# Kernel tuning notes

Hardware: AMD Instinct MI355X
Metric: run time of the kernel (lower is better)

Reference implementation:

```python
import jax, jax.numpy as jnp
import numpy as np

B, L, F = 32, 8192, 16
R, S = 32, 32            # residual / skip channels
NUM_BLOCKS, NUM_LAYERS = 3, 4
DILATIONS = [2 ** (i + j * NUM_LAYERS) for j in range(NUM_BLOCKS) for i in range(NUM_LAYERS)]  # 1..2048


def conv1d(x, w, b, dilation=1, padding=0):
    # x: (N, C, L), w: (O, I, K), matches torch Conv1d semantics
    y = jax.lax.conv_general_dilated(
        x, w, window_strides=(1,), padding=[(padding, padding)],
        rhs_dilation=(dilation,), dimension_numbers=("NCH", "OIH", "NCH"))
    return y + b[None, :, None]


def setup_inputs() -> dict:
    key = jax.random.key(0)
    ks = jax.random.split(key, 16)
    nl = NUM_BLOCKS * NUM_LAYERS
    sd = 0.1
    return {
        "x": jax.random.normal(ks[0], (B, L, F), dtype=jnp.float32),
        "in_w": sd * jax.random.normal(ks[1], (R, F, 1), dtype=jnp.float32),
        "in_b": jnp.zeros((R,), jnp.float32),
        "dil_w": sd * jax.random.normal(ks[2], (nl, 2 * R, R, 2), dtype=jnp.float32),
        "dil_b": jnp.zeros((nl, 2 * R), jnp.float32),
        "skip_w": sd * jax.random.normal(ks[3], (nl, S, R, 1), dtype=jnp.float32),
        "skip_b": jnp.zeros((nl, S), jnp.float32),
        "res_w": sd * jax.random.normal(ks[4], (nl, R, R, 1), dtype=jnp.float32),
        "res_b": jnp.zeros((nl, R), jnp.float32),
        "f1_w": sd * jax.random.normal(ks[5], (S, S, 1), dtype=jnp.float32),
        "f1_b": jnp.zeros((S,), jnp.float32),
        "f2_w": sd * jax.random.normal(ks[6], (1, S, 1), dtype=jnp.float32),
        "f2_b": jnp.zeros((1,), jnp.float32),
    }


def reference(x, in_w, in_b, dil_w, dil_b, skip_w, skip_b, res_w, res_b, f1_w, f1_b, f2_w, f2_b):
    # (B, L, F) -> (B, F, L)
    h = conv1d(jnp.transpose(x, (0, 2, 1)), in_w, in_b)
    skip_sum = None
    for l, d in enumerate(DILATIONS):
        residual = h
        y = conv1d(h, dil_w[l], dil_b[l], dilation=d, padding=d // 2)
        gate, filt = y[:, :R], y[:, R:]  # torch.chunk(dim=1)
        h = jnp.tanh(filt) * jax.nn.sigmoid(gate)
        s = conv1d(h, skip_w[l], skip_b[l])
        skip_sum = s if skip_sum is None else skip_sum + s
        h = conv1d(h, res_w[l], res_b[l])
        h = h + residual[:, :, -h.shape[2]:]  # causal trim (only layer 0 shrinks by 1)
    z = jax.nn.relu(skip_sum)
    z = jax.nn.relu(conv1d(z, f1_w, f1_b))
    z = conv1d(z, f2_w, f2_b)
    return z[:, 0, -1:]  # (B, 1)
```

## Files before the change

### kernel.cpp

```cpp
#include <hip/hip_runtime.h>
#include <hip/hip_bf16.h>


typedef __attribute__((ext_vector_type(8))) short short8;
typedef __attribute__((ext_vector_type(4))) float f32x4;

#define TLAST 8190
#define BATCH 32
#define MFMA(A, B, C) __builtin_amdgcn_mfma_f32_16x16x32_bf16(A, B, C, 0, 0, 0)

__device__ __forceinline__ ushort cvtb(float x) {
    union { __hip_bfloat16 b; ushort u; } c;
    c.b = __float2bfloat16(x);
    return c.u;
}
__device__ __forceinline__ float bf2f(ushort h) {
    return __uint_as_float((uint)h << 16);
}
__device__ __forceinline__ void split2(float v, ushort& h, ushort& l) {
    h = cvtb(v);
    l = cvtb(v - bf2f(h));
}
__device__ __forceinline__ int imin(int a, int b) { return a < b ? a : b; }
__device__ __forceinline__ float act_native(float gate, float filt) {
    const float e1 = __builtin_amdgcn_exp2f(filt * 2.885390082f);
    const float e2 = __builtin_amdgcn_exp2f(gate * -1.442695041f);
    return (e1 - 1.f) * __builtin_amdgcn_rcpf((e1 + 1.f) * (1.f + e2));
}

__global__ __launch_bounds__(256) void wn_prep(
    const float* __restrict__ dil_w, const float* __restrict__ res_w,
    ushort* __restrict__ Wd, ushort* __restrict__ Wr)
{
    const int idx = blockIdx.x * 256 + threadIdx.x;
    if (idx < 12 * 4096) {
        const int l = idx >> 12, rem = idx & 4095, n = rem >> 6, k = rem & 63;
        const int kt = k >> 5, ic = k & 31, o = (k >> 3) & 3, r8 = k & 7;
        const int lane = o * 16 + (n & 15), nt = n >> 4;
        const float v = dil_w[((size_t)l * 64 + n) * 64 + 2 * ic + kt];
        ushort h, lo;
        split2(v, h, lo);
        const int base = l * 8192 + ((kt * 4 + nt) * 2) * 512 + lane * 8 + r8;
        Wd[base] = h;
        Wd[base + 512] = lo;
    } else if (idx < 12 * 4096 + 12 * 1024) {
        const int j = idx - 12 * 4096;
        const int l = j >> 10, rem = j & 1023, n = rem >> 5, k = rem & 31;
        const int o = k >> 3, r8 = k & 7;
        const int lane = o * 16 + (n & 15), nt = n >> 4;
        ushort h, lo;
        split2(res_w[j], h, lo);
        const int base = l * 2048 + (nt * 2) * 512 + lane * 8 + r8;
        Wr[base] = h;
        Wr[base + 512] = lo;
    }
}

__global__ __launch_bounds__(256) void wn_fuseA(
    const float* __restrict__ x, const float* __restrict__ in_w,
    const float* __restrict__ in_b,
    const ushort* __restrict__ Wd, const ushort* __restrict__ Wr,
    const float* __restrict__ dil_b, const float* __restrict__ res_b,
    ushort* __restrict__ c6h, ushort* __restrict__ c6l,
    float* __restrict__ gTL)
{
    __shared__ __align__(16) ushort pingH[96 * 40], pingL[96 * 40];
    __shared__ __align__(16) ushort pongH[95 * 40], pongL[95 * 40];
    __shared__ __align__(16) ushort sGH[4][16 * 40], sGL[4][16 * 40];
    float* xs = (float*)pongH;

    const int tid = threadIdx.x, lane = tid & 63, w = tid >> 6;
    const int nl = lane & 15, o = lane >> 4;
    const int cc = blockIdx.x, b = blockIdx.y;
    const int t6a = 6174 + cc * 64, a0 = t6a - 31;
    const short8 z8 = {0, 0, 0, 0, 0, 0, 0, 0};

    for (int i = tid; i < 384; i += 256) {
        const int p = i >> 2, c4 = (i & 3) * 4;
        const int t = a0 + p;
        float4 v = make_float4(0.f, 0.f, 0.f, 0.f);
        if (t <= 8191) v = *(const float4*)&x[((size_t)b * 8192 + t) * 16 + c4];
        *(float4*)&xs[p * 20 + c4] = v;
    }
    __syncthreads();

    {
        const int c = tid & 31, pg = tid >> 5;
        float wr[16];
        #pragma unroll
        for (int f = 0; f < 16; ++f) wr[f] = in_w[c * 16 + f];
        const float bias = in_b[c];
        #pragma unroll
        for (int q = 0; q < 12; ++q) {
            const int p = pg + 8 * q;
            float acc = bias;
            #pragma unroll
            for (int f4 = 0; f4 < 4; ++f4) {
                const float4 xv = *(const float4*)&xs[p * 20 + f4 * 4];
                acc += wr[f4*4]*xv.x + wr[f4*4+1]*xv.y
                     + wr[f4*4+2]*xv.z + wr[f4*4+3]*xv.w;
            }
            ushort hh, hl;
            split2(acc, hh, hl);
            pingH[p * 40 + c] = hh;
            pingL[p * 40 + c] = hl;
        }
    }
    __syncthreads();

    for (int l = 0; l < 6; ++l) {
        const ushort* HiH = (l & 1) ? pongH : pingH;
        const ushort* HiL = (l & 1) ? pongL : pingL;
        ushort* HoH = (l & 1) ? pingH : pongH;
        ushort* HoL = (l & 1) ? pingL : pongL;
        const int nIn  = (l == 0) ? 96 : (192 >> l) - 1;
        const int nOut = (192 >> (l + 1)) - 1;
        const int nT   = (nOut + 15) >> 4;
        const int sO   = 1 << l;
        const int aO   = a0 + sO - 1;
        const int bOff = (l == 0) ? 1 : (sO >> 1);
        const int rmx  = (l == 0) ? 8191 : TLAST;
        const int first = (l == 0);
        const int capRem = TLAST - aO;
        const int capIdx = ((capRem % sO) == 0) ? (capRem / sO) : -1;

        const ushort* pd = Wd + (size_t)l * 8192;
        const ushort* pr = Wr + (size_t)l * 2048;
        float dbg[2], dbf[2], rbv[2];
        #pragma unroll
        for (int nt = 0; nt < 2; ++nt) {
            dbg[nt] = dil_b[l * 64 + nl + 16 * nt];
            dbf[nt] = dil_b[l * 64 + nl + 16 * nt + 32];
            rbv[nt] = res_b[l * 32 + nl + 16 * nt];
        }

        for (int tt = w; tt < nT; tt += 4) {
            const int joF = tt * 16 + nl;
            const int j0 = imin(first ? joF : 2 * joF, nIn - 1);
            const int j1 = imin(first ? joF + 1 : 2 * joF + 2, nIn - 1);
            const bool zB = (aO + joF * sO + bOff) > rmx;

            f32x4 aR[2];
            #pragma unroll
            for (int nt = 0; nt < 2; ++nt)
                #pragma unroll
                for (int r = 0; r < 4; ++r) {
                    const int joE = tt * 16 + 4 * o + r;
                    const int jres = imin(first ? joE + 1 : 2 * joE + 1, nIn - 1);
                    const int n = nl + 16 * nt;
                    aR[nt][r] = rbv[nt] + bf2f(HiH[jres * 40 + n]) +
                                bf2f(HiL[jres * 40 + n]);
                }

            short8 Ah[2], Al[2];
            Ah[0] = *(const short8*)&HiH[j0 * 40 + 8 * o];
            Al[0] = *(const short8*)&HiL[j0 * 40 + 8 * o];
            if (zB) { Ah[1] = z8; Al[1] = z8; }
            else {
                Ah[1] = *(const short8*)&HiH[j1 * 40 + 8 * o];
                Al[1] = *(const short8*)&HiL[j1 * 40 + 8 * o];
            }

            f32x4 acc[4];
            #pragma unroll
            for (int nt = 0; nt < 2; ++nt) {
                acc[nt]     = (f32x4){dbg[nt], dbg[nt], dbg[nt], dbg[nt]};
                acc[nt + 2] = (f32x4){dbf[nt], dbf[nt], dbf[nt], dbf[nt]};
            }
            #pragma unroll
            for (int kt = 0; kt < 2; ++kt)
                #pragma unroll
                for (int nt = 0; nt < 4; ++nt) {
                    const int base = ((kt * 4 + nt) * 2) * 512 + lane * 8;
                    const short8 Bh = *(const short8*)&pd[base];
                    const short8 Bl = *(const short8*)&pd[base + 512];
                    acc[nt] = MFMA(Ah[kt], Bh, acc[nt]);
                    acc[nt] = MFMA(Ah[kt], Bl, acc[nt]);
                    acc[nt] = MFMA(Al[kt], Bh, acc[nt]);
                }

            float gv[8];
            #pragma unroll
            for (int nt = 0; nt < 2; ++nt)
                #pragma unroll
                for (int r = 0; r < 4; ++r) {
                    const float g = act_native(acc[nt][r], acc[nt + 2][r]);
                    gv[nt * 4 + r] = g;
                    const int ml = 4 * o + r, n = nl + 16 * nt;
                    ushort gh16, gl16;
                    split2(g, gh16, gl16);
                    sGH[w][ml * 40 + n] = gh16;
                    sGL[w][ml * 40 + n] = gl16;
                }
            if (capIdx >= tt * 16 && capIdx < imin(tt * 16 + 16, nOut)) {
                #pragma unroll
                for (int nt = 0; nt < 2; ++nt)
                    #pragma unroll
                    for (int r = 0; r < 4; ++r)
                        if (tt * 16 + 4 * o + r == capIdx)
                            gTL[((size_t)l * BATCH + b) * 32 + nl + 16 * nt] =
                                gv[nt * 4 + r];
            }

            const short8 gh = *(const short8*)&sGH[w][nl * 40 + 8 * o];
            const short8 gl = *(const short8*)&sGL[w][nl * 40 + 8 * o];
            #pragma unroll
            for (int nt = 0; nt < 2; ++nt) {
                const int base = (nt * 2) * 512 + lane * 8;
                const short8 Rh = *(const short8*)&pr[base];
                const short8 Rl = *(const short8*)&pr[base + 512];
                aR[nt] = MFMA(gh, Rh, aR[nt]);
                aR[nt] = MFMA(gh, Rl, aR[nt]);
                aR[nt] = MFMA(gl, Rh, aR[nt]);
            }
            #pragma unroll
            for (int nt = 0; nt < 2; ++nt)
                #pragma unroll
                for (int r = 0; r < 4; ++r) {
                    const int joE = tt * 16 + 4 * o + r;
                    if (joE < nOut) {
                        const int n = nl + 16 * nt;
                        ushort hh, hl;
                        split2(aR[nt][r], hh, hl);
                        HoH[joE * 40 + n] = hh;
                        HoL[joE * 40 + n] = hl;
                        if (l == 5 && joE < 2) {
                            const size_t go = ((size_t)b * 64 + cc * 2 + joE) * 32 + n;
                            c6h[go] = hh;
                            c6l[go] = hl;
                        }
                    }
                }
        }
        __syncthreads();
    }
}

__device__ __forceinline__ void layer_tile1(
    const ushort* __restrict__ HiH, const ushort* __restrict__ HiL,
    ushort* __restrict__ HoH, ushort* __restrict__ HoL,
    const ushort* __restrict__ pd, const ushort* __restrict__ pr,
    const float* __restrict__ db, const float* __restrict__ rb,
    float* __restrict__ gout, ushort* __restrict__ sGH, ushort* __restrict__ sGL,
    int tt, int nIn, int nOut, int sO, int aO, int bOff,
    int lane, int nl, int o, int doRes)
{
    const short8 z8 = {0,0,0,0,0,0,0,0};
    const int joF = tt * 16 + nl;
    const int j0 = imin(2 * joF, nIn - 1);
    const int j1 = imin(2 * joF + 2, nIn - 1);
    const bool zB = (aO + joF * sO + bOff) > TLAST;

    float dbg[2], dbf[2], rbv[2];
    #pragma unroll
    for (int nt = 0; nt < 2; ++nt) {
        dbg[nt] = db[nl + 16 * nt];
        dbf[nt] = db[nl + 16 * nt + 32];
        rbv[nt] = rb[nl + 16 * nt];
    }

    f32x4 aR[2];
    #pragma unroll
    for (int nt = 0; nt < 2; ++nt)
        #pragma unroll
        for (int r = 0; r < 4; ++r) {
            const int joE = tt * 16 + 4 * o + r;
            const int jres = imin(2 * joE + 1, nIn - 1);
            const int n = nl + 16 * nt;
            aR[nt][r] = rbv[nt] + bf2f(HiH[jres * 40 + n]) +
                        bf2f(HiL[jres * 40 + n]);
        }

    short8 Ah[2], Al[2];
    Ah[0] = *(const short8*)&HiH[j0 * 40 + 8 * o];
    Al[0] = *(const short8*)&HiL[j0 * 40 + 8 * o];
    if (zB) { Ah[1] = z8; Al[1] = z8; }
    else {
        Ah[1] = *(const short8*)&HiH[j1 * 40 + 8 * o];
        Al[1] = *(const short8*)&HiL[j1 * 40 + 8 * o];
    }

    f32x4 acc[4];
    #pragma unroll
    for (int nt = 0; nt < 2; ++nt) {
        acc[nt]     = (f32x4){dbg[nt], dbg[nt], dbg[nt], dbg[nt]};
        acc[nt + 2] = (f32x4){dbf[nt], dbf[nt], dbf[nt], dbf[nt]};
    }
    #pragma unroll
    for (int kt = 0; kt < 2; ++kt)
        #pragma unroll
        for (int nt = 0; nt < 4; ++nt) {
            const int base = ((kt * 4 + nt) * 2) * 512 + lane * 8;
            const short8 Bh = *(const short8*)&pd[base];
            const short8 Bl = *(const short8*)&pd[base + 512];
            acc[nt] = MFMA(Ah[kt], Bh, acc[nt]);
            acc[nt] = MFMA(Ah[kt], Bl, acc[nt]);
            acc[nt] = MFMA(Al[kt], Bh, acc[nt]);
        }

    const int capRem = TLAST - aO;
    const int capIdx = ((capRem % sO) == 0) ? (capRem / sO) : -1;
    float gv[8];
    #pragma unroll
    for (int nt = 0; nt < 2; ++nt)
        #pragma unroll
        for (int r = 0; r < 4; ++r) {
            const float g = act_native(acc[nt][r], acc[nt + 2][r]);
            gv[nt * 4 + r] = g;
            const int ml = 4 * o + r, n = nl + 16 * nt;
            ushort gh16, gl16;
            split2(g, gh16, gl16);
            sGH[ml * 40 + n] = gh16;
            sGL[ml * 40 + n] = gl16;
        }
    if (capIdx >= tt * 16 && capIdx < imin(tt * 16 + 16, nOut)) {
        #pragma unroll
        for (int nt = 0; nt < 2; ++nt)
            #pragma unroll
            for (int r = 0; r < 4; ++r)
                if (tt * 16 + 4 * o + r == capIdx)
                    gout[nl + 16 * nt] = gv[nt * 4 + r];
    }

    if (doRes) {
        const short8 gh = *(const short8*)&sGH[nl * 40 + 8 * o];
        const short8 gl = *(const short8*)&sGL[nl * 40 + 8 * o];
        #pragma unroll
        for (int nt = 0; nt < 2; ++nt) {
            const int base = (nt * 2) * 512 + lane * 8;
            const short8 Rh = *(const short8*)&pr[base];
            const short8 Rl = *(const short8*)&pr[base + 512];
            aR[nt] = MFMA(gh, Rh, aR[nt]);
            aR[nt] = MFMA(gh, Rl, aR[nt]);
            aR[nt] = MFMA(gl, Rh, aR[nt]);
        }
        #pragma unroll
        for (int nt = 0; nt < 2; ++nt)
            #pragma unroll
            for (int r = 0; r < 4; ++r) {
                const int joE = tt * 16 + 4 * o + r;
                if (joE < nOut) {
                    const int n = nl + 16 * nt;
                    ushort hh, hl;
                    split2(aR[nt][r], hh, hl);
                    HoH[joE * 40 + n] = hh;
                    HoL[joE * 40 + n] = hl;
                }
            }
    }
}

__global__ __launch_bounds__(256) void wn_fuseB(
    const ushort* __restrict__ c6h, const ushort* __restrict__ c6l,
    const ushort* __restrict__ Wd, const ushort* __restrict__ Wr,
    const float* __restrict__ dil_b, const float* __restrict__ res_b,
    const float* __restrict__ gTL,
    const float* __restrict__ sw, const float* __restrict__ sb,
    const float* __restrict__ f1w, const float* __restrict__ f1b,
    const float* __restrict__ f2w, const float* __restrict__ f2b,
    float* __restrict__ out)
{
    __shared__ __align__(16) ushort HAh[64 * 40], HAl[64 * 40];
    __shared__ __align__(16) ushort HBh[32 * 40], HBl[32 * 40];
    __shared__ __align__(16) ushort sG2H[2][16 * 40], sG2L[2][16 * 40];
    __shared__ float gcap[6 * 32];
    __shared__ float psum[4][32];
    __shared__ float hd[64];

    const int tid = threadIdx.x, lane = tid & 63, w = tid >> 6;
    const int nl = lane & 15, o = lane >> 4;
    const int b = blockIdx.x;

    for (int i = tid; i < 256; i += 256) {
        const int row = i >> 2, c8 = (i & 3) * 8;
        *(short8*)&HAh[row * 40 + c8] = *(const short8*)&c6h[((size_t)b * 64 + row) * 32 + c8];
        *(short8*)&HAl[row * 40 + c8] = *(const short8*)&c6l[((size_t)b * 64 + row) * 32 + c8];
    }
    __syncthreads();

    if (w < 2) {
        layer_tile1(HAh, HAl, HBh, HBl, Wd + 6 * 8192, Wr + 6 * 2048,
                    dil_b + 6 * 64, res_b + 6 * 32,
                    gcap, sG2H[w], sG2L[w],
                    w, 64, 32, 64, 6206, 32, lane, nl, o, 1);
    }
    __syncthreads();

    if (w == 0) {
        for (int ll = 1; ll < 6; ++ll) {
            const int l = ll + 6;
            const ushort* HiH = (ll & 1) ? HBh : HAh;
            const ushort* HiL = (ll & 1) ? HBl : HAl;
            ushort* HoH = (ll & 1) ? HAh : HBh;
            ushort* HoL = (ll & 1) ? HAl : HBl;
            const int sO = 64 << ll;
            layer_tile1(HiH, HiL, HoH, HoL,
                        Wd + (size_t)l * 8192, Wr + (size_t)l * 2048,
                        dil_b + l * 64, res_b + l * 32,
                        gcap + ll * 32, sG2H[0], sG2L[0],
                        0, 64 >> ll, 32 >> ll, sO, 6142 + sO, sO >> 1,
                        lane, nl, o, (ll < 5) ? 1 : 0);
        }
    }
    __syncthreads();

    if (lane < 32) {
        const int c = lane;
        float part = 0.f;
        #pragma unroll
        for (int j = 0; j < 3; ++j) {
            const int l2 = 3 * w + j;
            float a = sb[l2 * 32 + c];
            const float* swr = sw + l2 * 1024 + c * 32;
            const float* gvp = (l2 < 6) ? (gTL + ((size_t)l2 * BATCH + b) * 32)
                                        : (gcap + (l2 - 6) * 32);
            #pragma unroll
            for (int ic = 0; ic < 32; ++ic) a += swr[ic] * gvp[ic];
            part += a;
        }
        psum[w][c] = part;
    }
    __syncthreads();

    if (w == 0 && lane < 32)
        hd[lane] = fmaxf(psum[0][lane] + psum[1][lane] + psum[2][lane] + psum[3][lane], 0.f);
    if (w == 0 && lane < 32) {
        float z = f1b[lane];
        #pragma unroll
        for (int ic = 0; ic < 32; ++ic) z += f1w[lane * 32 + ic] * hd[ic];
        hd[32 + lane] = fmaxf(z, 0.f);
    }
    if (w == 0 && lane == 0) {
        float o2 = f2b[0];
        #pragma unroll
        for (int ic = 0; ic < 32; ++ic) o2 += f2w[ic] * hd[32 + ic];
        out[b] = o2;
    }
}

extern "C" void kernel_launch(void* const* d_in, const int* in_sizes, int n_in,
                              void* d_out, int out_size, void* d_ws, size_t ws_size,
                              hipStream_t stream)
{
    const float* x      = (const float*)d_in[0];
    const float* in_w   = (const float*)d_in[1];
    const float* in_b   = (const float*)d_in[2];
    const float* dil_w  = (const float*)d_in[3];
    const float* dil_b  = (const float*)d_in[4];
    const float* skip_w = (const float*)d_in[5];
    const float* skip_b = (const float*)d_in[6];
    const float* res_w  = (const float*)d_in[7];
    const float* res_b  = (const float*)d_in[8];
    const float* f1_w   = (const float*)d_in[9];
    const float* f1_b   = (const float*)d_in[10];
    const float* f2_w   = (const float*)d_in[11];
    const float* f2_b   = (const float*)d_in[12];

    char* p = (char*)d_ws;
    ushort* Wd  = (ushort*)p; p += 12 * 8192 * 2;
    ushort* Wr  = (ushort*)p; p += 12 * 2048 * 2;
    ushort* c6h = (ushort*)p; p += 32 * 64 * 32 * 2;
    ushort* c6l = (ushort*)p; p += 32 * 64 * 32 * 2;
    float*  gTL = (float*)p;

    wn_prep<<<dim3(240), dim3(256), 0, stream>>>(dil_w, res_w, Wd, Wr);

    wn_fuseA<<<dim3(32, BATCH), dim3(256), 0, stream>>>(
        x, in_w, in_b, Wd, Wr, dil_b, res_b, c6h, c6l, gTL);

    wn_fuseB<<<dim3(BATCH), dim3(256), 0, stream>>>(
        c6h, c6l, Wd, Wr, dil_b, res_b, gTL,
        skip_w, skip_b, f1_w, f1_b, f2_w, f2_b, (float*)d_out);
}
```

Before: 59.01 us.

## Load residual via identity-matrix MFMA and double fuseA block to 512 threads

The residual gather, previously eight scalar LDS loads per n-tile with bf16-to-float conversion, is replaced by two vector short8 loads per tile. These are transposed into the MFMA accumulator layout by multiplying against identity fragments. Separately, wn_fuseA now runs 512 threads (8 waves) per block with per-wave staging buffers doubled, so each wave processes fewer tiles. The cost is four extra MFMAs per tile and higher LDS use per block, which may reduce occupancy.

After: 62.19 us. +5.4%, slower.

```diff
diff --git a/kernel.cpp b/kernel.cpp
--- a/kernel.cpp
+++ b/kernel.cpp
@@ -26,6 +26,13 @@
     const float e1 = __builtin_amdgcn_exp2f(filt * 2.885390082f);
     const float e2 = __builtin_amdgcn_exp2f(gate * -1.442695041f);
     return (e1 - 1.f) * __builtin_amdgcn_rcpf((e1 + 1.f) * (1.f + e2));
+}
+__device__ __forceinline__ short8 ident_frag(int nl, int o, int nt) {
+    short8 v = {0, 0, 0, 0, 0, 0, 0, 0};
+    #pragma unroll
+    for (int j = 0; j < 8; ++j)
+        v[j] = (8 * o + j == nl + 16 * nt) ? (short)0x3F80 : (short)0;
+    return v;
 }
 
 __global__ __launch_bounds__(256) void wn_prep(
@@ -56,7 +63,7 @@
     }
 }
 
-__global__ __launch_bounds__(256) void wn_fuseA(
+__global__ __launch_bounds__(512) void wn_fuseA(
     const float* __restrict__ x, const float* __restrict__ in_w,
     const float* __restrict__ in_b,
     const ushort* __restrict__ Wd, const ushort* __restrict__ Wr,
@@ -66,7 +73,7 @@
 {
     __shared__ __align__(16) ushort pingH[96 * 40], pingL[96 * 40];
     __shared__ __align__(16) ushort pongH[95 * 40], pongL[95 * 40];
-    __shared__ __align__(16) ushort sGH[4][16 * 40], sGL[4][16 * 40];
+    __shared__ __align__(16) ushort sGH[8][16 * 40], sGL[8][16 * 40];
     float* xs = (float*)pongH;
 
     const int tid = threadIdx.x, lane = tid & 63, w = tid >> 6;
@@ -74,8 +81,10 @@
     const int cc = blockIdx.x, b = blockIdx.y;
     const int t6a = 6174 + cc * 64, a0 = t6a - 31;
     const short8 z8 = {0, 0, 0, 0, 0, 0, 0, 0};
-
-    for (int i = tid; i < 384; i += 256) {
+    const short8 I0 = ident_frag(nl, o, 0);
+    const short8 I1 = ident_frag(nl, o, 1);
+
+    for (int i = tid; i < 384; i += 512) {
         const int p = i >> 2, c4 = (i & 3) * 4;
         const int t = a0 + p;
         float4 v = make_float4(0.f, 0.f, 0.f, 0.f);
@@ -91,8 +100,8 @@
         for (int f = 0; f < 16; ++f) wr[f] = in_w[c * 16 + f];
         const float bias = in_b[c];
         #pragma unroll
-        for (int q = 0; q < 12; ++q) {
-            const int p = pg + 8 * q;
+        for (int q = 0; q < 6; ++q) {
+            const int p = pg + 16 * q;
             float acc = bias;
             #pragma unroll
             for (int f4 = 0; f4 < 4; ++f4) {
@@ -134,23 +143,22 @@
             rbv[nt] = res_b[l * 32 + nl + 16 * nt];
         }
 
-        for (int tt = w; tt < nT; tt += 4) {
+        for (int tt = w; tt < nT; tt += 8) {
             const int joF = tt * 16 + nl;
             const int j0 = imin(first ? joF : 2 * joF, nIn - 1);
             const int j1 = imin(first ? joF + 1 : 2 * joF + 2, nIn - 1);
+            const int jr = imin(first ? joF + 1 : 2 * joF + 1, nIn - 1);
             const bool zB = (aO + joF * sO + bOff) > rmx;
 
+            const short8 RhA = *(const short8*)&HiH[jr * 40 + 8 * o];
+            const short8 RlA = *(const short8*)&HiL[jr * 40 + 8 * o];
             f32x4 aR[2];
-            #pragma unroll
-            for (int nt = 0; nt < 2; ++nt)
-                #pragma unroll
-                for (int r = 0; r < 4; ++r) {
-                    const int joE = tt * 16 + 4 * o + r;
-                    const int jres = imin(first ? joE + 1 : 2 * joE + 1, nIn - 1);
-                    const int n = nl + 16 * nt;
-                    aR[nt][r] = rbv[nt] + bf2f(HiH[jres * 40 + n]) +
-                                bf2f(HiL[jres * 40 + n]);
-                }
+            aR[0] = (f32x4){rbv[0], rbv[0], rbv[0], rbv[0]};
+            aR[1] = (f32x4){rbv[1], rbv[1], rbv[1], rbv[1]};
+            aR[0] = MFMA(RhA, I0, aR[0]);
+            aR[0] = MFMA(RlA, I0, aR[0]);
+            aR[1] = MFMA(RhA, I1, aR[1]);
+            aR[1] = MFMA(RlA, I1, aR[1]);
 
             short8 Ah[2], Al[2];
             Ah[0] = *(const short8*)&HiH[j0 * 40 + 8 * o];
@@ -249,6 +257,7 @@
     const int joF = tt * 16 + nl;
     const int j0 = imin(2 * joF, nIn - 1);
     const int j1 = imin(2 * joF + 2, nIn - 1);
+    const int jr = imin(2 * joF + 1, nIn - 1);
     const bool zB = (aO + joF * sO + bOff) > TLAST;
 
     float dbg[2], dbf[2], rbv[2];
@@ -259,17 +268,17 @@
         rbv[nt] = rb[nl + 16 * nt];
     }
 
+    const short8 I0 = ident_frag(nl, o, 0);
+    const short8 I1 = ident_frag(nl, o, 1);
+    const short8 RhA = *(const short8*)&HiH[jr * 40 + 8 * o];
+    const short8 RlA = *(const short8*)&HiL[jr * 40 + 8 * o];
     f32x4 aR[2];
-    #pragma unroll
-    for (int nt = 0; nt < 2; ++nt)
-        #pragma unroll
-        for (int r = 0; r < 4; ++r) {
-            const int joE = tt * 16 + 4 * o + r;
-            const int jres = imin(2 * joE + 1, nIn - 1);
-            const int n = nl + 16 * nt;
-            aR[nt][r] = rbv[nt] + bf2f(HiH[jres * 40 + n]) +
-                        bf2f(HiL[jres * 40 + n]);
-        }
+    aR[0] = (f32x4){rbv[0], rbv[0], rbv[0], rbv[0]};
+    aR[1] = (f32x4){rbv[1], rbv[1], rbv[1], rbv[1]};
+    aR[0] = MFMA(RhA, I0, aR[0]);
+    aR[0] = MFMA(RlA, I0, aR[0]);
+    aR[1] = MFMA(RhA, I1, aR[1]);
+    aR[1] = MFMA(RlA, I1, aR[1]);
 
     short8 Ah[2], Al[2];
     Ah[0] = *(const short8*)&HiH[j0 * 40 + 8 * o];
@@ -465,7 +474,7 @@
 
     wn_prep<<<dim3(240), dim3(256), 0, stream>>>(dil_w, res_w, Wd, Wr);
 
-    wn_fuseA<<<dim3(32, BATCH), dim3(256), 0, stream>>>(
+    wn_fuseA<<<dim3(32, BATCH), dim3(512), 0, stream>>>(
         x, in_w, in_b, Wd, Wr, dil_b, res_b, c6h, c6l, gTL);
 
     wn_fuseB<<<dim3(BATCH), dim3(256), 0, stream>>>(
```
